# Performance work log

Hardware: AMD Instinct MI355X
Metric: run time of the kernel (lower is better)

Reference implementation:

```python
import jax, jax.numpy as jnp
import numpy as np

B, S, D, F, E = 8, 2048, 768, 3072, 8
EPS = 1e-6


def setup_inputs() -> dict:
    key = jax.random.key(0)
    k1, k2, k3, k4 = jax.random.split(key, 4)
    return {
        "hidden_states": jax.random.normal(k1, (B, S, D), dtype=jnp.float32),
        "ln_weight": jnp.ones((D,), dtype=jnp.float32),
        "router_w": jax.random.normal(k2, (D, E), dtype=jnp.float32) * (D ** -0.5),
        "wi": jax.random.normal(k3, (E, D, F), dtype=jnp.float32) * 0.02,
        "wo": jax.random.normal(k4, (E, F, D), dtype=jnp.float32) * 0.02,
        "output_router_logits": 1,
    }


def reference(hidden_states, ln_weight, router_w, wi, wo, output_router_logits):
    # T5-style RMS layer norm (no mean subtraction, no bias)
    var = jnp.mean(jnp.square(hidden_states), axis=-1, keepdims=True)
    x = hidden_states * jax.lax.rsqrt(var + EPS) * ln_weight  # [B,S,D]

    # Top-1 router: linear (no bias) -> softmax -> argmax
    router_logits = jnp.einsum("bsd,de->bse", x, router_w)        # [B,S,E]
    router_probs = jax.nn.softmax(router_logits, axis=-1)
    expert_index = jnp.argmax(router_probs, axis=-1)              # [B,S] int
    top_prob = jnp.max(router_probs, axis=-1, keepdims=True)      # [B,S,1]

    # Dispatch: each token processed by its argmax expert (masked combine)
    next_states = jnp.zeros_like(x)
    n_exp = router_w.shape[-1]
    for e in range(n_exp):
        h = jax.nn.relu(jnp.einsum("bsd,df->bsf", x, wi[e]))
        y = jnp.einsum("bsf,fd->bsd", h, wo[e])
        next_states = next_states + jnp.where((expert_index == e)[..., None], y, 0.0)

    # Probability-weighted combine + residual (dropout is identity at eval)
    output = hidden_states + top_prob * next_states
    if output_router_logits:
        return (output, router_logits, expert_index)
    return output
```

## Files before the change

kernel.cpp:

```cpp
#include <hip/hip_runtime.h>
#include <math.h>

#define N_TOK 16384
#define DIM   768
#define FFD   3072
#define NEXP  8
#define EPSV  1e-6f

typedef __attribute__((ext_vector_type(4))) float f32x4;
typedef __attribute__((ext_vector_type(4))) unsigned short u16x4;
typedef __attribute__((ext_vector_type(8))) unsigned short u16x8;
typedef __attribute__((ext_vector_type(8))) __bf16 bf16x8;

static __device__ __forceinline__ unsigned short f2bf(float f) {
    unsigned int u = __builtin_bit_cast(unsigned int, f);
    u += 0x7fffu + ((u >> 16) & 1u);
    return (unsigned short)(u >> 16);
}
static __device__ __forceinline__ bf16x8 as_bf(u16x8 v) {
    return __builtin_bit_cast(bf16x8, v);
}
static __device__ __forceinline__ void gload16(const void* g, void* l) {
    __builtin_amdgcn_global_load_lds(
        (const __attribute__((address_space(1))) unsigned int*)g,
        (__attribute__((address_space(3))) unsigned int*)l, 16, 0, 0);
}

__global__ __launch_bounds__(256) void k_setup(
    const float* __restrict__ wi, unsigned short* __restrict__ wib,
    const float* __restrict__ wo, unsigned short* __restrict__ wob,
    const float* __restrict__ x, const float* __restrict__ lnw,
    const float* __restrict__ rw,
    float* __restrict__ out_logits, float* __restrict__ out_eidx,
    float* __restrict__ topp, int* __restrict__ eidx,
    unsigned short* __restrict__ xn)
{
    __shared__ float tile[64][65];
    const int t = threadIdx.x;
    const int b = blockIdx.x;

    if (b < 9216) {
        const float* in;
        unsigned short* outp;
        int R, C, bb;
        if (b < 4608) { in = wi; outp = wib; R = DIM; C = FFD; bb = b; }
        else          { in = wo; outp = wob; R = FFD; C = DIM; bb = b - 4608; }
        const int bc = C >> 6, br = R >> 6;
        const int e = bb / (bc * br);
        const int rem = bb - e * bc * br;
        const int rt = rem / bc, ct = rem - rt * bc;
        {
            const int r = t >> 2, c4 = (t & 3) << 4;
            const float* src = in + ((size_t)e * R + rt * 64 + r) * C + ct * 64 + c4;
#pragma unroll
            for (int q = 0; q < 4; q++) {
                float4 f = ((const float4*)src)[q];
                tile[r][c4 + q * 4 + 0] = f.x;
                tile[r][c4 + q * 4 + 1] = f.y;
                tile[r][c4 + q * 4 + 2] = f.z;
                tile[r][c4 + q * 4 + 3] = f.w;
            }
        }
        __syncthreads();
        {
            const int c = t >> 2, r4 = (t & 3) << 4;
            u16x8 o0, o1;
#pragma unroll
            for (int j = 0; j < 8; j++)  o0[j] = f2bf(tile[r4 + j][c]);
#pragma unroll
            for (int j = 0; j < 8; j++)  o1[j] = f2bf(tile[r4 + 8 + j][c]);
            unsigned short* dst = outp + ((size_t)e * C + ct * 64 + c) * R + rt * 64 + r4;
            *(u16x8*)dst       = o0;
            *(u16x8*)(dst + 8) = o1;
        }
        return;
    }

    const int wid = t >> 6, lane = t & 63;
    const int tok = (b - 9216) * 4 + wid;
    const size_t base = (size_t)tok * DIM;
    float* xvs = ((float*)tile) + wid * 768;

    float4 v[3];
#pragma unroll
    for (int j = 0; j < 3; j++)
        v[j] = *(const float4*)(x + base + lane * 4 + j * 256);
    float ss = 0.f;
#pragma unroll
    for (int j = 0; j < 3; j++)
        ss += v[j].x * v[j].x + v[j].y * v[j].y + v[j].z * v[j].z + v[j].w * v[j].w;
#pragma unroll
    for (int s = 32; s > 0; s >>= 1) ss += __shfl_xor(ss, s);
    const float rstd = rsqrtf(ss * (1.0f / DIM) + EPSV);

#pragma unroll
    for (int j = 0; j < 3; j++) {
        float4 lw = *(const float4*)(lnw + lane * 4 + j * 256);
        float xv0 = v[j].x * rstd * lw.x, xv1 = v[j].y * rstd * lw.y;
        float xv2 = v[j].z * rstd * lw.z, xv3 = v[j].w * rstd * lw.w;
        u16x4 pk = { f2bf(xv0), f2bf(xv1), f2bf(xv2), f2bf(xv3) };
        *(u16x4*)(xn + base + lane * 4 + j * 256) = pk;
        float4 xq = { xv0, xv1, xv2, xv3 };
        *(float4*)&xvs[lane * 4 + j * 256] = xq;
    }
    __syncthreads();

    float rp = 0.f;
#pragma unroll 8
    for (int q = 0; q < 96; q++) {
        float xvv = xvs[(lane >> 3) + q * 8];
        float rwv = rw[q * 64 + lane];
        rp = fmaf(xvv, rwv, rp);
    }
    rp += __shfl_xor(rp, 8);
    rp += __shfl_xor(rp, 16);
    rp += __shfl_xor(rp, 32);
    if (lane < 8) out_logits[(size_t)tok * 8 + lane] = rp;

    float mx = rp; int am = lane & 7;
#pragma unroll
    for (int s = 1; s < 8; s <<= 1) {
        float o = __shfl_xor(mx, s);
        int  oa = __shfl_xor(am, s);
        if (o > mx || (o == mx && oa < am)) { mx = o; am = oa; }
    }
    float se = expf(rp - mx);
    se += __shfl_xor(se, 1);
    se += __shfl_xor(se, 2);
    se += __shfl_xor(se, 4);
    if (lane == 0) {
        topp[tok] = 1.0f / se;
        out_eidx[tok] = (float)am;
        eidx[tok] = am;
    }
}

__global__ __launch_bounds__(256) void k_hist(
    const int* __restrict__ eidx, int* __restrict__ blkhist)
{
    __shared__ int h[8];
    if (threadIdx.x < 8) h[threadIdx.x] = 0;
    __syncthreads();
    atomicAdd(&h[eidx[blockIdx.x * 256 + threadIdx.x]], 1);
    __syncthreads();
    if (threadIdx.x < 8) blkhist[blockIdx.x * 8 + threadIdx.x] = h[threadIdx.x];
}

__global__ __launch_bounds__(512) void k_prefix(
    const int* __restrict__ blkhist, int* __restrict__ base,
    int* __restrict__ cnt)
{
    __shared__ int h[64 * 8];
    __shared__ int tot[8];
    __shared__ int eb[8];
    const int t = threadIdx.x;
    h[t] = blkhist[t];
    __syncthreads();
    const int b = t >> 3, e = t & 7;
    int s = 0;
    for (int bb = 0; bb < b; bb++) s += h[bb * 8 + e];
    if (b == 63) tot[e] = s + h[63 * 8 + e];
    __syncthreads();
    if (t == 0) {
        int p = 0;
#pragma unroll
        for (int q = 0; q < 8; q++) { eb[q] = p; p += tot[q]; }
    }
    __syncthreads();
    base[t] = eb[e] + s;
    if (t < 8) cnt[t] = tot[t];
}

__global__ __launch_bounds__(256) void k_scatter(
    const int* __restrict__ eidx, const int* __restrict__ base,
    int* __restrict__ list)
{
    __shared__ int wcnt[4][8];
    __shared__ int bb[8];
    const int t = threadIdx.x, b = blockIdx.x;
    const int lane = t & 63, wid = t >> 6;
    if (t < 8) bb[t] = base[b * 8 + t];
    const int tok = b * 256 + t;
    const int e = eidx[tok];
    int wrank = 0;
#pragma unroll
    for (int q = 0; q < 8; q++) {
        unsigned long long m = __ballot(e == q);
        if (e == q) wrank = __popcll(m & ((1ull << lane) - 1ull));
        if (lane == 0) wcnt[wid][q] = __popcll(m);
    }
    __syncthreads();
    int wbase = 0;
#pragma unroll
    for (int w = 0; w < 4; w++)
        if (w < wid) wbase += wcnt[w][e];
    list[bb[e] + wbase + wrank] = tok;
}

__global__ __launch_bounds__(256, 2) void k_gemm1(
    const unsigned short* __restrict__ A, const unsigned short* __restrict__ Bw,
    const int* __restrict__ list, const int* __restrict__ cnt,
    unsigned short* __restrict__ Hout)
{
    constexpr int K   = DIM;
    constexpr int N   = FFD;
    constexpr int TNT = N / 256;
    __shared__ unsigned short Asm[128 * 64];
    __shared__ unsigned short Bsm[256 * 64];
    __shared__ int tokrow[128];
    __shared__ int spref[9];
    __shared__ int ebase[8];

    const int t = threadIdx.x, lane = t & 63, wid = t >> 6;
    if (t == 0) {
        int p = 0, qq = 0;
        spref[0] = 0;
#pragma unroll
        for (int e = 0; e < 8; e++) {
            ebase[e] = qq; qq += cnt[e];
            p += (cnt[e] + 127) >> 7;
            spref[e + 1] = p;
        }
    }
    __syncthreads();
    const int total = spref[8] * TNT;
    const int moff = (wid >> 1) * 64, noff = (wid & 1) * 128;
    const int lr = lane & 15, lq = lane >> 4;

    const int nwg = gridDim.x;
    const int xcd = blockIdx.x & 7, rr8 = blockIdx.x >> 3;
    const int qd = nwg >> 3, rm = nwg & 7;
    const int bid = (xcd < rm ? xcd * (qd + 1) : rm * (qd + 1) + (xcd - rm) * qd) + rr8;

    int arow[4], asub[4], brow[8], bsub[8];
#pragma unroll
    for (int i = 0; i < 4; i++) {
        int c = (wid * 4 + i) * 64 + lane;
        arow[i] = c >> 3;
        asub[i] = (c & 7) ^ (arow[i] & 7);
    }
#pragma unroll
    for (int i = 0; i < 8; i++) {
        int c = (wid * 8 + i) * 64 + lane;
        brow[i] = c >> 3;
        bsub[i] = (c & 7) ^ (brow[i] & 7);
    }

    for (int w = bid; w < total; w += gridDim.x) {
        const int gm = w / TNT, tn = w - gm * TNT;
        int e = 0;
        while (gm >= spref[e + 1]) e++;
        const int ce = cnt[e], eb = ebase[e];
        const int m0 = (gm - spref[e]) * 128, n0 = tn * 256;

        __syncthreads();
        if (t < 128)
            tokrow[t] = (m0 + t < ce) ? list[eb + m0 + t] : list[eb];
        __syncthreads();

        const unsigned short* aP[4];
        const unsigned short* bP[8];
#pragma unroll
        for (int i = 0; i < 4; i++)
            aP[i] = A + (size_t)tokrow[arow[i]] * K + asub[i] * 8;
#pragma unroll
        for (int i = 0; i < 8; i++)
            bP[i] = Bw + ((size_t)e * N + n0 + brow[i]) * K + bsub[i] * 8;

        f32x4 acc[4][8];
#pragma unroll
        for (int mi = 0; mi < 4; mi++)
#pragma unroll
            for (int ni = 0; ni < 8; ni++) acc[mi][ni] = (f32x4){0, 0, 0, 0};

        for (int k0 = 0; k0 < K; k0 += 64) {
#pragma unroll
            for (int i = 0; i < 4; i++)
                gload16(aP[i] + k0, Asm + (wid * 4 + i) * 512);
#pragma unroll
            for (int i = 0; i < 8; i++)
                gload16(bP[i] + k0, Bsm + (wid * 8 + i) * 512);
            __syncthreads();
#pragma unroll
            for (int kf = 0; kf < 2; kf++) {
                const int phys = ((kf * 4 + lq) ^ (lr & 7)) * 8;
                bf16x8 af[4], bfr[8];
#pragma unroll
                for (int mi = 0; mi < 4; mi++)
                    af[mi] = as_bf(*(const u16x8*)&Asm[(moff + mi * 16 + lr) * 64 + phys]);
#pragma unroll
                for (int ni = 0; ni < 8; ni++)
                    bfr[ni] = as_bf(*(const u16x8*)&Bsm[(noff + ni * 16 + lr) * 64 + phys]);
#pragma unroll
                for (int mi = 0; mi < 4; mi++)
#pragma unroll
                    for (int ni = 0; ni < 8; ni++)
                        acc[mi][ni] = __builtin_amdgcn_mfma_f32_16x16x32_bf16(
                            af[mi], bfr[ni], acc[mi][ni], 0, 0, 0);
            }
            __syncthreads();
        }

#pragma unroll
        for (int mi = 0; mi < 4; mi++) {
#pragma unroll
            for (int r4 = 0; r4 < 4; r4++) {
                const int row = moff + mi * 16 + lq * 4 + r4;
                if (m0 + row < ce) {
                    unsigned short* hp = Hout + (size_t)(eb + m0 + row) * FFD + n0 + noff;
#pragma unroll
                    for (int ni = 0; ni < 8; ni++) {
                        float v = acc[mi][ni][r4];
                        v = v > 0.f ? v : 0.f;
                        hp[ni * 16 + lr] = f2bf(v);
                    }
                }
            }
        }
    }
}

__global__ __launch_bounds__(256, 2) void k_gemm2(
    const unsigned short* __restrict__ A, const unsigned short* __restrict__ Bw,
    const int* __restrict__ list, const int* __restrict__ cnt,
    const float* __restrict__ hs, const float* __restrict__ topp,
    float* __restrict__ out)
{
    constexpr int K   = FFD;
    constexpr int N   = DIM;
    constexpr int TNT = N / 256;
    __shared__ unsigned short Asm[128 * 64];
    __shared__ unsigned short Bsm[256 * 64];
    __shared__ int tokrow[128];
    __shared__ int spref[9];
    __shared__ int ebase[8];

    const int t = threadIdx.x, lane = t & 63, wid = t >> 6;
    if (t == 0) {
        int p = 0, qq = 0;
        spref[0] = 0;
#pragma unroll
        for (int e = 0; e < 8; e++) {
            ebase[e] = qq; qq += cnt[e];
            p += (cnt[e] + 127) >> 7;
            spref[e + 1] = p;
        }
    }
    __syncthreads();
    const int total = spref[8] * TNT;
    const int moff = (wid >> 1) * 64, noff = (wid & 1) * 128;
    const int lr = lane & 15, lq = lane >> 4;

    const int nwg = gridDim.x;
    const int xcd = blockIdx.x & 7, rr8 = blockIdx.x >> 3;
    const int qd = nwg >> 3, rm = nwg & 7;
    const int bid = (xcd < rm ? xcd * (qd + 1) : rm * (qd + 1) + (xcd - rm) * qd) + rr8;

    int arow[4], asub[4], brow[8], bsub[8];
#pragma unroll
    for (int i = 0; i < 4; i++) {
        int c = (wid * 4 + i) * 64 + lane;
        arow[i] = c >> 3;
        asub[i] = (c & 7) ^ (arow[i] & 7);
    }
#pragma unroll
    for (int i = 0; i < 8; i++) {
        int c = (wid * 8 + i) * 64 + lane;
        brow[i] = c >> 3;
        bsub[i] = (c & 7) ^ (brow[i] & 7);
    }

    for (int w = bid; w < total; w += gridDim.x) {
        const int gm = w / TNT, tn = w - gm * TNT;
        int e = 0;
        while (gm >= spref[e + 1]) e++;
        const int ce = cnt[e], eb = ebase[e];
        const int m0 = (gm - spref[e]) * 128, n0 = tn * 256;

        __syncthreads();
        if (t < 128)
            tokrow[t] = (m0 + t < ce) ? list[eb + m0 + t] : list[eb];
        __syncthreads();

        const unsigned short* aP[4];
        const unsigned short* bP[8];
#pragma unroll
        for (int i = 0; i < 4; i++) {
            const int drow = (m0 + arow[i] < ce) ? (m0 + arow[i]) : (ce - 1);
            aP[i] = A + (size_t)(eb + drow) * K + asub[i] * 8;
        }
#pragma unroll
        for (int i = 0; i < 8; i++)
            bP[i] = Bw + ((size_t)e * N + n0 + brow[i]) * K + bsub[i] * 8;

        f32x4 acc[4][8];
#pragma unroll
        for (int mi = 0; mi < 4; mi++)
#pragma unroll
            for (int ni = 0; ni < 8; ni++) acc[mi][ni] = (f32x4){0, 0, 0, 0};

        for (int k0 = 0; k0 < K; k0 += 64) {
#pragma unroll
            for (int i = 0; i < 4; i++)
                gload16(aP[i] + k0, Asm + (wid * 4 + i) * 512);
#pragma unroll
            for (int i = 0; i < 8; i++)
                gload16(bP[i] + k0, Bsm + (wid * 8 + i) * 512);
            __syncthreads();
#pragma unroll
            for (int kf = 0; kf < 2; kf++) {
                const int phys = ((kf * 4 + lq) ^ (lr & 7)) * 8;
                bf16x8 af[4], bfr[8];
#pragma unroll
                for (int mi = 0; mi < 4; mi++)
                    af[mi] = as_bf(*(const u16x8*)&Asm[(moff + mi * 16 + lr) * 64 + phys]);
#pragma unroll
                for (int ni = 0; ni < 8; ni++)
                    bfr[ni] = as_bf(*(const u16x8*)&Bsm[(noff + ni * 16 + lr) * 64 + phys]);
#pragma unroll
                for (int mi = 0; mi < 4; mi++)
#pragma unroll
                    for (int ni = 0; ni < 8; ni++)
                        acc[mi][ni] = __builtin_amdgcn_mfma_f32_16x16x32_bf16(
                            af[mi], bfr[ni], acc[mi][ni], 0, 0, 0);
            }
            __syncthreads();
        }

#pragma unroll
        for (int mi = 0; mi < 4; mi++) {
#pragma unroll
            for (int r4 = 0; r4 < 4; r4++) {
                const int row = moff + mi * 16 + lq * 4 + r4;
                if (m0 + row < ce) {
                    const int tok = tokrow[row];
                    const float tp = topp[tok];
#pragma unroll
                    for (int ni = 0; ni < 8; ni++) {
                        const size_t idx = (size_t)tok * DIM + n0 + noff + ni * 16 + lr;
                        out[idx] = hs[idx] + tp * acc[mi][ni][r4];
                    }
                }
            }
        }
    }
}

extern "C" void kernel_launch(void* const* d_in, const int* in_sizes, int n_in,
                              void* d_out, int out_size, void* d_ws, size_t ws_size,
                              hipStream_t stream)
{
    const float* hs  = (const float*)d_in[0];
    const float* lnw = (const float*)d_in[1];
    const float* rw  = (const float*)d_in[2];
    const float* wi  = (const float*)d_in[3];
    const float* wo  = (const float*)d_in[4];

    float* out        = (float*)d_out;
    float* out_logits = out + (size_t)N_TOK * DIM;
    float* out_eidx   = out_logits + (size_t)N_TOK * NEXP;

    char* ws = (char*)d_ws;
    size_t off = 0;
    int*   cnt     = (int*)(ws + off);         off += 256;
    int*   list    = (int*)(ws + off);         off += (size_t)N_TOK * 4;
    float* topp    = (float*)(ws + off);       off += (size_t)N_TOK * 4;
    int*   eidx    = (int*)(ws + off);         off += (size_t)N_TOK * 4;
    int*   blkhist = (int*)(ws + off);         off += 4096;
    int*   base    = (int*)(ws + off);         off += 4096;
    unsigned short* xn  = (unsigned short*)(ws + off); off += (size_t)N_TOK * DIM * 2;
    unsigned short* Hb  = (unsigned short*)(ws + off); off += (size_t)N_TOK * FFD * 2;
    unsigned short* wob = (unsigned short*)(ws + off);

    unsigned short* wib = (unsigned short*)d_out;

    k_setup<<<13312, 256, 0, stream>>>(wi, wib, wo, wob, hs, lnw, rw,
                                       out_logits, out_eidx, topp, eidx, xn);
    k_hist<<<64, 256, 0, stream>>>(eidx, blkhist);
    k_prefix<<<1, 512, 0, stream>>>(blkhist, base, cnt);
    k_scatter<<<64, 256, 0, stream>>>(eidx, base, list);
    k_gemm1<<<1632, 256, 0, stream>>>(xn, wib, list, cnt, Hb);
    k_gemm2<<<408, 256, 0, stream>>>(Hb, wob, list, cnt, hs, topp, out);
}
```

Measured before the change: 274.6 us.

## Fuse expert GEMM1 and GEMM2 into persistent work-queue kernel with per-tile flags

Replaces the two separate expert GEMM launches with one persistent kernel of 512 blocks. Blocks pull work items from an atomic queue: first all up-projection tiles, then down-projection tiles. Each down-projection tile spins on a per-row-block flag until its 12 up-projection tiles have published their outputs. This lets the second GEMM overlap the tail of the first and removes a launch boundary, at the cost of atomics, spin-waiting, and moving the bf16 wi copy into the workspace. The fused path runs only when the workspace is large enough; otherwise the old two-kernel path is used.

New measurement: 353.6 us. 28.8% more time.

```diff
diff --git a/kernel.cpp b/kernel.cpp
--- a/kernel.cpp
+++ b/kernel.cpp
@@ -148,13 +148,15 @@
 
 __global__ __launch_bounds__(512) void k_prefix(
     const int* __restrict__ blkhist, int* __restrict__ base,
-    int* __restrict__ cnt)
+    int* __restrict__ cnt, int* __restrict__ wq, int* __restrict__ flag)
 {
     __shared__ int h[64 * 8];
     __shared__ int tot[8];
     __shared__ int eb[8];
     const int t = threadIdx.x;
     h[t] = blkhist[t];
+    if (t == 0) *wq = 0;
+    if (t < 256) flag[t] = 0;
     __syncthreads();
     const int b = t >> 3, e = t & 7;
     int s = 0;
@@ -197,6 +199,173 @@
     list[bb[e] + wbase + wrank] = tok;
 }
 
+__global__ __launch_bounds__(256, 2) void k_ffn(
+    const unsigned short* __restrict__ xn, const unsigned short* __restrict__ wib,
+    const unsigned short* __restrict__ wob, unsigned short* __restrict__ Hb,
+    const int* __restrict__ list, const int* __restrict__ cnt,
+    const float* __restrict__ hs, const float* __restrict__ topp,
+    float* __restrict__ out, int* __restrict__ wq, int* __restrict__ flag)
+{
+    __shared__ unsigned short Asm[128 * 64];
+    __shared__ unsigned short Bsm[256 * 64];
+    __shared__ int tokrow[128];
+    __shared__ int spref[9];
+    __shared__ int ebase[8];
+    __shared__ int sitem;
+
+    const int t = threadIdx.x, lane = t & 63, wid = t >> 6;
+    if (t == 0) {
+        int p = 0, qq = 0;
+        spref[0] = 0;
+#pragma unroll
+        for (int e = 0; e < 8; e++) {
+            ebase[e] = qq; qq += cnt[e];
+            p += (cnt[e] + 127) >> 7;
+            spref[e + 1] = p;
+        }
+    }
+    __syncthreads();
+    const int nmt = spref[8];
+    const int total1 = nmt * 12;
+    const int total  = total1 + nmt * 3;
+    const int moff = (wid >> 1) * 64, noff = (wid & 1) * 128;
+    const int lr = lane & 15, lq = lane >> 4;
+
+    int arow[4], asub[4], brow[8], bsub[8];
+#pragma unroll
+    for (int i = 0; i < 4; i++) {
+        int c = (wid * 4 + i) * 64 + lane;
+        arow[i] = c >> 3;
+        asub[i] = (c & 7) ^ (arow[i] & 7);
+    }
+#pragma unroll
+    for (int i = 0; i < 8; i++) {
+        int c = (wid * 8 + i) * 64 + lane;
+        brow[i] = c >> 3;
+        bsub[i] = (c & 7) ^ (brow[i] & 7);
+    }
+
+    for (;;) {
+        __syncthreads();
+        if (t == 0) sitem = atomicAdd(wq, 1);
+        __syncthreads();
+        const int item = sitem;
+        if (item >= total) break;
+
+        const bool g1 = (item < total1);
+        const int it2 = g1 ? item : item - total1;
+        const int per = g1 ? 12 : 3;
+        const int gm = it2 / per, tn = it2 - gm * per;
+        int e = 0;
+        while (gm >= spref[e + 1]) e++;
+        const int ce = cnt[e], eb = ebase[e];
+        const int m0 = (gm - spref[e]) * 128, n0 = tn * 256;
+        const int K = g1 ? DIM : FFD;
+        const int BN = g1 ? FFD : DIM;
+
+        if (!g1 && t == 0) {
+            while (__hip_atomic_load(flag + gm, __ATOMIC_RELAXED,
+                                     __HIP_MEMORY_SCOPE_AGENT) < 12)
+                __builtin_amdgcn_s_sleep(8);
+            (void)__hip_atomic_load(flag + gm, __ATOMIC_ACQUIRE,
+                                    __HIP_MEMORY_SCOPE_AGENT);
+        }
+        if (t < 128)
+            tokrow[t] = (m0 + t < ce) ? list[eb + m0 + t] : list[eb];
+        __syncthreads();
+
+        const unsigned short* aP[4];
+        const unsigned short* bP[8];
+        const unsigned short* Bw = g1 ? wib : wob;
+#pragma unroll
+        for (int i = 0; i < 4; i++) {
+            if (g1) {
+                aP[i] = xn + (size_t)tokrow[arow[i]] * DIM + asub[i] * 8;
+            } else {
+                const int drow = (m0 + arow[i] < ce) ? (m0 + arow[i]) : (ce - 1);
+                aP[i] = Hb + (size_t)(eb + drow) * FFD + asub[i] * 8;
+            }
+        }
+#pragma unroll
+        for (int i = 0; i < 8; i++)
+            bP[i] = Bw + ((size_t)e * BN + n0 + brow[i]) * K + bsub[i] * 8;
+
+        f32x4 acc[4][8];
+#pragma unroll
+        for (int mi = 0; mi < 4; mi++)
+#pragma unroll
+            for (int ni = 0; ni < 8; ni++) acc[mi][ni] = (f32x4){0, 0, 0, 0};
+
+        for (int k0 = 0; k0 < K; k0 += 64) {
+#pragma unroll
+            for (int i = 0; i < 4; i++)
+                gload16(aP[i] + k0, Asm + (wid * 4 + i) * 512);
+#pragma unroll
+            for (int i = 0; i < 8; i++)
+                gload16(bP[i] + k0, Bsm + (wid * 8 + i) * 512);
+            __syncthreads();
+#pragma unroll
+            for (int kf = 0; kf < 2; kf++) {
+                const int phys = ((kf * 4 + lq) ^ (lr & 7)) * 8;
+                bf16x8 af[4], bfr[8];
+#pragma unroll
+                for (int mi = 0; mi < 4; mi++)
+                    af[mi] = as_bf(*(const u16x8*)&Asm[(moff + mi * 16 + lr) * 64 + phys]);
+#pragma unroll
+                for (int ni = 0; ni < 8; ni++)
+                    bfr[ni] = as_bf(*(const u16x8*)&Bsm[(noff + ni * 16 + lr) * 64 + phys]);
+#pragma unroll
+                for (int mi = 0; mi < 4; mi++)
+#pragma unroll
+                    for (int ni = 0; ni < 8; ni++)
+                        acc[mi][ni] = __builtin_amdgcn_mfma_f32_16x16x32_bf16(
+                            af[mi], bfr[ni], acc[mi][ni], 0, 0, 0);
+            }
+            __syncthreads();
+        }
+
+        if (g1) {
+#pragma unroll
+            for (int mi = 0; mi < 4; mi++) {
+#pragma unroll
+                for (int r4 = 0; r4 < 4; r4++) {
+                    const int row = moff + mi * 16 + lq * 4 + r4;
+                    if (m0 + row < ce) {
+                        unsigned short* hp = Hb + (size_t)(eb + m0 + row) * FFD + n0 + noff;
+#pragma unroll
+                        for (int ni = 0; ni < 8; ni++) {
+                            float v = acc[mi][ni][r4];
+                            v = v > 0.f ? v : 0.f;
+                            hp[ni * 16 + lr] = f2bf(v);
+                        }
+                    }
+                }
+            }
+            __syncthreads();
+            if (t == 0)
+                __hip_atomic_fetch_add(flag + gm, 1, __ATOMIC_RELEASE,
+                                       __HIP_MEMORY_SCOPE_AGENT);
+        } else {
+#pragma unroll
+            for (int mi = 0; mi < 4; mi++) {
+#pragma unroll
+                for (int r4 = 0; r4 < 4; r4++) {
+                    const int row = moff + mi * 16 + lq * 4 + r4;
+                    if (m0 + row < ce) {
+                        const int tok = tokrow[row];
+                        const float tp = topp[tok];
+#pragma unroll
+                        for (int ni = 0; ni < 8; ni++) {
+                            const size_t idx = (size_t)tok * DIM + n0 + noff + ni * 16 + lr;
+                            out[idx] = hs[idx] + tp * acc[mi][ni][r4];
+                        }
+                    }
+                }
+            }
+        }
+    }
+}
+
 __global__ __launch_bounds__(256, 2) void k_gemm1(
     const unsigned short* __restrict__ A, const unsigned short* __restrict__ Bw,
     const int* __restrict__ list, const int* __restrict__ cnt,
@@ -468,17 +637,27 @@
     int*   eidx    = (int*)(ws + off);         off += (size_t)N_TOK * 4;
     int*   blkhist = (int*)(ws + off);         off += 4096;
     int*   base    = (int*)(ws + off);         off += 4096;
+    int*   wq      = (int*)(ws + off);
+    int*   flag    = wq + 16;                  off += 4096;
     unsigned short* xn  = (unsigned short*)(ws + off); off += (size_t)N_TOK * DIM * 2;
     unsigned short* Hb  = (unsigned short*)(ws + off); off += (size_t)N_TOK * FFD * 2;
-    unsigned short* wob = (unsigned short*)(ws + off);
-
-    unsigned short* wib = (unsigned short*)d_out;
+    unsigned short* wob = (unsigned short*)(ws + off); off += (size_t)NEXP * FFD * DIM * 2;
+    unsigned short* wib_ws = (unsigned short*)(ws + off);
+    const size_t need = off + (size_t)NEXP * FFD * DIM * 2;
+    const bool fused = (ws_size >= need);
+
+    unsigned short* wib = fused ? wib_ws : (unsigned short*)d_out;
 
     k_setup<<<13312, 256, 0, stream>>>(wi, wib, wo, wob, hs, lnw, rw,
                                        out_logits, out_eidx, topp, eidx, xn);
     k_hist<<<64, 256, 0, stream>>>(eidx, blkhist);
-    k_prefix<<<1, 512, 0, stream>>>(blkhist, base, cnt);
+    k_prefix<<<1, 512, 0, stream>>>(blkhist, base, cnt, wq, flag);
     k_scatter<<<64, 256, 0, stream>>>(eidx, base, list);
-    k_gemm1<<<1632, 256, 0, stream>>>(xn, wib, list, cnt, Hb);
-    k_gemm2<<<408, 256, 0, stream>>>(Hb, wob, list, cnt, hs, topp, out);
-}
+    if (fused) {
+        k_ffn<<<512, 256, 0, stream>>>(xn, wib, wob, Hb, list, cnt,
+                                       hs, topp, out, wq, flag);
+    } else {
+        k_gemm1<<<1632, 256, 0, stream>>>(xn, wib, list, cnt, Hb);
+        k_gemm2<<<408, 256, 0, stream>>>(Hb, wob, list, cnt, hs, topp, out);
+    }
+}
```

## Overlap wo bf16 transpose with gemm1 and fold prefix into scatter

Applied to the files above, without the earlier changes.

The wo fp32-to-bf16 transpose moves out of the setup kernel and into extra trailing workgroups of the first grouped GEMM launch, so it can run alongside GEMM work instead of serialising before routing. The single-block prefix kernel is removed and each scatter block recomputes the per-expert totals and offsets from the block histograms, dropping one launch. Risks include the transpose blocks competing with GEMM tiles for CUs and bandwidth. The XCD remapping is now hard-coded to the 1632-block GEMM grid.

Result: faster. 265.5 us (median of 2 runs) (-3.3%).

```diff
diff --git a/kernel.cpp b/kernel.cpp
--- a/kernel.cpp
+++ b/kernel.cpp
@@ -28,7 +28,6 @@
 
 __global__ __launch_bounds__(256) void k_setup(
     const float* __restrict__ wi, unsigned short* __restrict__ wib,
-    const float* __restrict__ wo, unsigned short* __restrict__ wob,
     const float* __restrict__ x, const float* __restrict__ lnw,
     const float* __restrict__ rw,
     float* __restrict__ out_logits, float* __restrict__ out_eidx,
@@ -39,19 +38,14 @@
     const int t = threadIdx.x;
     const int b = blockIdx.x;
 
-    if (b < 9216) {
-        const float* in;
-        unsigned short* outp;
-        int R, C, bb;
-        if (b < 4608) { in = wi; outp = wib; R = DIM; C = FFD; bb = b; }
-        else          { in = wo; outp = wob; R = FFD; C = DIM; bb = b - 4608; }
-        const int bc = C >> 6, br = R >> 6;
-        const int e = bb / (bc * br);
-        const int rem = bb - e * bc * br;
+    if (b < 4608) {
+        const int bc = FFD >> 6, br = DIM >> 6;
+        const int e = b / (bc * br);
+        const int rem = b - e * bc * br;
         const int rt = rem / bc, ct = rem - rt * bc;
         {
             const int r = t >> 2, c4 = (t & 3) << 4;
-            const float* src = in + ((size_t)e * R + rt * 64 + r) * C + ct * 64 + c4;
+            const float* src = wi + ((size_t)e * DIM + rt * 64 + r) * FFD + ct * 64 + c4;
 #pragma unroll
             for (int q = 0; q < 4; q++) {
                 float4 f = ((const float4*)src)[q];
@@ -69,7 +63,7 @@
             for (int j = 0; j < 8; j++)  o0[j] = f2bf(tile[r4 + j][c]);
 #pragma unroll
             for (int j = 0; j < 8; j++)  o1[j] = f2bf(tile[r4 + 8 + j][c]);
-            unsigned short* dst = outp + ((size_t)e * C + ct * 64 + c) * R + rt * 64 + r4;
+            unsigned short* dst = wib + ((size_t)e * FFD + ct * 64 + c) * DIM + rt * 64 + r4;
             *(u16x8*)dst       = o0;
             *(u16x8*)(dst + 8) = o1;
         }
@@ -77,7 +71,7 @@
     }
 
     const int wid = t >> 6, lane = t & 63;
-    const int tok = (b - 9216) * 4 + wid;
+    const int tok = (b - 4608) * 4 + wid;
     const size_t base = (size_t)tok * DIM;
     float* xvs = ((float*)tile) + wid * 768;
 
@@ -146,40 +140,33 @@
     if (threadIdx.x < 8) blkhist[blockIdx.x * 8 + threadIdx.x] = h[threadIdx.x];
 }
 
-__global__ __launch_bounds__(512) void k_prefix(
-    const int* __restrict__ blkhist, int* __restrict__ base,
-    int* __restrict__ cnt)
+__global__ __launch_bounds__(256) void k_scatter(
+    const int* __restrict__ eidx, const int* __restrict__ blkhist,
+    int* __restrict__ list, int* __restrict__ cnt)
 {
     __shared__ int h[64 * 8];
     __shared__ int tot[8];
-    __shared__ int eb[8];
-    const int t = threadIdx.x;
-    h[t] = blkhist[t];
-    __syncthreads();
-    const int b = t >> 3, e = t & 7;
-    int s = 0;
-    for (int bb = 0; bb < b; bb++) s += h[bb * 8 + e];
-    if (b == 63) tot[e] = s + h[63 * 8 + e];
-    __syncthreads();
-    if (t == 0) {
-        int p = 0;
-#pragma unroll
-        for (int q = 0; q < 8; q++) { eb[q] = p; p += tot[q]; }
-    }
-    __syncthreads();
-    base[t] = eb[e] + s;
-    if (t < 8) cnt[t] = tot[t];
-}
-
-__global__ __launch_bounds__(256) void k_scatter(
-    const int* __restrict__ eidx, const int* __restrict__ base,
-    int* __restrict__ list)
-{
+    __shared__ int bb8[8];
     __shared__ int wcnt[4][8];
-    __shared__ int bb[8];
     const int t = threadIdx.x, b = blockIdx.x;
     const int lane = t & 63, wid = t >> 6;
-    if (t < 8) bb[t] = base[b * 8 + t];
+    h[t] = blkhist[t];
+    h[t + 256] = blkhist[t + 256];
+    __syncthreads();
+    if (t < 8) {
+        int s = 0;
+        for (int q = 0; q < 64; q++) s += h[q * 8 + t];
+        tot[t] = s;
+    }
+    __syncthreads();
+    if (t < 8) {
+        int eb = 0;
+        for (int q = 0; q < t; q++) eb += tot[q];
+        int sp = 0;
+        for (int q = 0; q < b; q++) sp += h[q * 8 + t];
+        bb8[t] = eb + sp;
+        if (b == 0) cnt[t] = tot[t];
+    }
     const int tok = b * 256 + t;
     const int e = eidx[tok];
     int wrank = 0;
@@ -194,17 +181,19 @@
 #pragma unroll
     for (int w = 0; w < 4; w++)
         if (w < wid) wbase += wcnt[w][e];
-    list[bb[e] + wbase + wrank] = tok;
+    list[bb8[e] + wbase + wrank] = tok;
 }
 
 __global__ __launch_bounds__(256, 2) void k_gemm1(
     const unsigned short* __restrict__ A, const unsigned short* __restrict__ Bw,
     const int* __restrict__ list, const int* __restrict__ cnt,
-    unsigned short* __restrict__ Hout)
+    unsigned short* __restrict__ Hout,
+    const float* __restrict__ wo, unsigned short* __restrict__ wob)
 {
     constexpr int K   = DIM;
     constexpr int N   = FFD;
     constexpr int TNT = N / 256;
+    constexpr int NWG = 1632;
     __shared__ unsigned short Asm[128 * 64];
     __shared__ unsigned short Bsm[256 * 64];
     __shared__ int tokrow[128];
@@ -212,6 +201,41 @@
     __shared__ int ebase[8];
 
     const int t = threadIdx.x, lane = t & 63, wid = t >> 6;
+
+    if (blockIdx.x >= NWG) {
+        float (*tile)[65] = reinterpret_cast<float(*)[65]>(Bsm);
+        const int bb = blockIdx.x - NWG;
+        const int bc = DIM >> 6, br = FFD >> 6;
+        const int e = bb / (bc * br);
+        const int rem = bb - e * bc * br;
+        const int rt = rem / bc, ct = rem - rt * bc;
+        {
+            const int r = t >> 2, c4 = (t & 3) << 4;
+            const float* src = wo + ((size_t)e * FFD + rt * 64 + r) * DIM + ct * 64 + c4;
+#pragma unroll
+            for (int q = 0; q < 4; q++) {
+                float4 f = ((const float4*)src)[q];
+                tile[r][c4 + q * 4 + 0] = f.x;
+                tile[r][c4 + q * 4 + 1] = f.y;
+                tile[r][c4 + q * 4 + 2] = f.z;
+                tile[r][c4 + q * 4 + 3] = f.w;
+            }
+        }
+        __syncthreads();
+        {
+            const int c = t >> 2, r4 = (t & 3) << 4;
+            u16x8 o0, o1;
+#pragma unroll
+            for (int j = 0; j < 8; j++)  o0[j] = f2bf(tile[r4 + j][c]);
+#pragma unroll
+            for (int j = 0; j < 8; j++)  o1[j] = f2bf(tile[r4 + 8 + j][c]);
+            unsigned short* dst = wob + ((size_t)e * DIM + ct * 64 + c) * FFD + rt * 64 + r4;
+            *(u16x8*)dst       = o0;
+            *(u16x8*)(dst + 8) = o1;
+        }
+        return;
+    }
+
     if (t == 0) {
         int p = 0, qq = 0;
         spref[0] = 0;
@@ -227,10 +251,8 @@
     const int moff = (wid >> 1) * 64, noff = (wid & 1) * 128;
     const int lr = lane & 15, lq = lane >> 4;
 
-    const int nwg = gridDim.x;
     const int xcd = blockIdx.x & 7, rr8 = blockIdx.x >> 3;
-    const int qd = nwg >> 3, rm = nwg & 7;
-    const int bid = (xcd < rm ? xcd * (qd + 1) : rm * (qd + 1) + (xcd - rm) * qd) + rr8;
+    const int bid = xcd * (NWG >> 3) + rr8;
 
     int arow[4], asub[4], brow[8], bsub[8];
 #pragma unroll
@@ -246,7 +268,7 @@
         bsub[i] = (c & 7) ^ (brow[i] & 7);
     }
 
-    for (int w = bid; w < total; w += gridDim.x) {
+    for (int w = bid; w < total; w += NWG) {
         const int gm = w / TNT, tn = w - gm * TNT;
         int e = 0;
         while (gm >= spref[e + 1]) e++;
@@ -467,18 +489,16 @@
     float* topp    = (float*)(ws + off);       off += (size_t)N_TOK * 4;
     int*   eidx    = (int*)(ws + off);         off += (size_t)N_TOK * 4;
     int*   blkhist = (int*)(ws + off);         off += 4096;
-    int*   base    = (int*)(ws + off);         off += 4096;
     unsigned short* xn  = (unsigned short*)(ws + off); off += (size_t)N_TOK * DIM * 2;
     unsigned short* Hb  = (unsigned short*)(ws + off); off += (size_t)N_TOK * FFD * 2;
     unsigned short* wob = (unsigned short*)(ws + off);
 
     unsigned short* wib = (unsigned short*)d_out;
 
-    k_setup<<<13312, 256, 0, stream>>>(wi, wib, wo, wob, hs, lnw, rw,
-                                       out_logits, out_eidx, topp, eidx, xn);
+    k_setup<<<8704, 256, 0, stream>>>(wi, wib, hs, lnw, rw,
+                                      out_logits, out_eidx, topp, eidx, xn);
     k_hist<<<64, 256, 0, stream>>>(eidx, blkhist);
-    k_prefix<<<1, 512, 0, stream>>>(blkhist, base, cnt);
-    k_scatter<<<64, 256, 0, stream>>>(eidx, base, list);
-    k_gemm1<<<1632, 256, 0, stream>>>(xn, wib, list, cnt, Hb);
+    k_scatter<<<64, 256, 0, stream>>>(eidx, blkhist, list, cnt);
+    k_gemm1<<<6240, 256, 0, stream>>>(xn, wib, list, cnt, Hb, wo, wob);
     k_gemm2<<<408, 256, 0, stream>>>(Hb, wob, list, cnt, hs, topp, out);
 }
```
